# Kernel optimization log

Hardware: AMD Instinct MI355X
Metric: run time of the kernel (lower is better)

The kernel has to match this reference:

```python
import jax, jax.numpy as jnp
import numpy as np


def _window_indices(L, K):
    # 0-based (emo, cau) index pairs kept in the torch flattening order:
    # emo varies slowly (outer), cau varies fast (inner), |cau-emo| <= K.
    i = np.repeat(np.arange(L), L)
    j = np.tile(np.arange(L), L)
    m = np.abs(j - i) <= K
    return i[m], j[m]


def setup_inputs() -> dict:
    key = jax.random.key(0)
    ks = jax.random.split(key, 6)
    B, L, D = 4, 512, 768
    K, P = 10, 50
    R = 2 * D + P  # rank_feat_dim = 1586
    return {
        "doc_sents_h": jax.random.normal(ks[0], (B, L, D), jnp.float32),
        "pos_emb": jax.random.normal(ks[1], (2 * K + 1, P), jnp.float32) * 0.05,
        "W1": jax.random.normal(ks[2], (R, R), jnp.float32) * (1.0 / np.sqrt(R)),
        "b1": jax.random.normal(ks[3], (R,), jnp.float32) * 0.01,
        "W2": jax.random.normal(ks[4], (R, 1), jnp.float32) * (1.0 / np.sqrt(R)),
        "b2": jax.random.normal(ks[5], (1,), jnp.float32) * 0.01,
    }


def reference(doc_sents_h, pos_emb, W1, b1, W2, b2):
    B, L, D = doc_sents_h.shape
    K = (pos_emb.shape[0] - 1) // 2
    ei, ci = _window_indices(L, K)           # static numpy, shape [n]
    rel = jnp.asarray(ci - ei)               # [n] in [-K, K]
    # windowed pair features, [B, n, 2D] (skips the O(L^2) materialization)
    P_pairs = jnp.concatenate([doc_sents_h[:, ei], doc_sents_h[:, ci]], axis=-1)
    emb = pos_emb[rel + K]                   # [n, pos_dim]
    relf = rel.astype(pos_emb.dtype)
    kernel = jnp.exp(-jnp.square(relf[:, None] - relf[None, :]))  # [n, n]
    emb = kernel @ emb                       # [n, pos_dim], batch-invariant
    couples = jnp.concatenate(
        [P_pairs, jnp.broadcast_to(emb, (B,) + emb.shape)], axis=-1)  # [B, n, R]
    h = jax.nn.relu(couples @ W1 + b1)       # [B, n, R]
    pred = (h @ W2 + b2)[..., 0]             # [B, n]
    emo_cau_pos = jnp.stack(
        [jnp.asarray(ei) + 1, jnp.asarray(ci) + 1], axis=1)  # [n, 2], 1-based
    return pred, emo_cau_pos, h
```

## Files before the change

### kernel.cpp

```cpp
#include <hip/hip_runtime.h>
#include <math.h>

#define B_   4
#define L_   512
#define D_   768
#define K_   10
#define P_   50
#define R_   1586
#define NP_  10642
#define MROWS 2048
#define NPAD 1664
#define UVS  1600

#define PRED_OFF 0
#define POS_OFF  (B_ * NP_)
#define H_OFF    (B_ * NP_ + NP_ * 2)

typedef __attribute__((ext_vector_type(8))) short short8;
typedef __attribute__((ext_vector_type(4))) float floatx4;

__device__ __forceinline__ unsigned short f2bf(float f) {
    union { float f; unsigned int u; } a; a.f = f;
    unsigned int u = a.u;
    return (unsigned short)((u + 0x7FFF + ((u >> 16) & 1)) >> 16);
}
__device__ __forceinline__ float bf2f(unsigned short u) {
    union { unsigned int u; float f; } a; a.u = ((unsigned int)u) << 16;
    return a.f;
}

__device__ __forceinline__ int pair_offset(int i) {
    int h = i < K_ ? i : K_;
    int off = h * (K_ + 1) + (h * (h - 1)) / 2;
    if (i > K_) {
        int fullEnd = i < (L_ - K_) ? i : (L_ - K_);
        off += (fullEnd - K_) * (2 * K_ + 1);
        if (i > L_ - K_) {
            int t = i - (L_ - K_);
            int first = 2 * K_;
            int last = L_ + K_ - (i - 1);
            off += (first + last) * t / 2;
        }
    }
    return off;
}

__global__ __launch_bounds__(256) void convert_A(
        const float* __restrict__ doc, unsigned short* __restrict__ At) {
    int idx = (blockIdx.x * 256 + threadIdx.x) * 4;
    float4 v = *(const float4*)(doc + idx);
    ushort4 o;
    o.x = f2bf(v.x); o.y = f2bf(v.y); o.z = f2bf(v.z); o.w = f2bf(v.w);
    *(ushort4*)(At + idx) = o;
}

__global__ __launch_bounds__(256) void convert_W(
        const float* __restrict__ W1, unsigned short* __restrict__ Wt) {
    int z = blockIdx.z;
    int k0 = blockIdx.x * 32;
    int n0 = blockIdx.y * 32;
    __shared__ float tile[32][33];
    int tx = threadIdx.x & 31, ty = threadIdx.x >> 5;
    #pragma unroll
    for (int r = 0; r < 4; ++r) {
        int k = k0 + ty + r * 8;
        int n = n0 + tx;
        tile[ty + r * 8][tx] = (n < R_) ? W1[(size_t)(z * D_ + k) * R_ + n] : 0.f;
    }
    __syncthreads();
    #pragma unroll
    for (int r = 0; r < 4; ++r) {
        int n = n0 + ty + r * 8;
        int k = k0 + tx;
        Wt[(size_t)z * NPAD * D_ + (size_t)n * D_ + k] = f2bf(tile[tx][ty + r * 8]);
    }
}

__global__ __launch_bounds__(256) void build_F(
        const float* __restrict__ pos_emb, const float* __restrict__ W1,
        const float* __restrict__ b1, unsigned short* __restrict__ Fb) {
    int s = blockIdx.x;
    __shared__ float Es[P_];
    if (threadIdx.x < P_) {
        float acc = 0.f;
        #pragma unroll
        for (int r = 0; r <= 2 * K_; ++r) {
            float cnt = (float)(L_ - (r > K_ ? r - K_ : K_ - r));
            float d = (float)(s - r);
            acc += cnt * expf(-d * d) * pos_emb[r * P_ + threadIdx.x];
        }
        Es[threadIdx.x] = acc;
    }
    __syncthreads();
    for (int j = threadIdx.x; j < R_; j += blockDim.x) {
        float acc = b1[j];
        #pragma unroll 10
        for (int p = 0; p < P_; ++p)
            acc += Es[p] * W1[(2 * D_ + p) * R_ + j];
        Fb[s * UVS + j] = f2bf(acc);
    }
}

#define GLOAD_LDS16(g, l) __builtin_amdgcn_global_load_lds( \
    (const __attribute__((address_space(1))) void*)(g), \
    (__attribute__((address_space(3))) void*)(l), 16, 0, 0)

__global__ __launch_bounds__(256) void gemm_mfma(
        const unsigned short* __restrict__ At,
        const unsigned short* __restrict__ Wt,
        unsigned short* __restrict__ U, unsigned short* __restrict__ V) {
    __shared__ unsigned short Alds[128 * 32];
    __shared__ unsigned short Blds[128 * 32];
    const int tileN = blockIdx.x * 128;
    const int tileM = blockIdx.y * 128;
    const unsigned short* Bt = Wt + (size_t)blockIdx.z * NPAD * D_;
    unsigned short* C = blockIdx.z ? V : U;

    const int lane = threadIdx.x & 63;
    const int w = threadIdx.x >> 6;
    const int wm = (w & 1) * 64, wn = (w >> 1) * 64;
    const int quad = lane >> 4, l16 = lane & 15;

    floatx4 acc[4][4] = {};

    for (int k0 = 0; k0 < D_; k0 += 32) {
        #pragma unroll
        for (int t = 0; t < 2; ++t) {
            int g = (t * 4 + w) * 64 + lane;
            int m = g >> 2, c = g & 3;
            GLOAD_LDS16(At + (size_t)(tileM + m) * D_ + k0 + c * 8,
                        Alds + (t * 4 + w) * 512);
            GLOAD_LDS16(Bt + (size_t)(tileN + m) * D_ + k0 + c * 8,
                        Blds + (t * 4 + w) * 512);
        }
        __syncthreads();
        short8 a[4], b[4];
        #pragma unroll
        for (int im = 0; im < 4; ++im)
            a[im] = *(const short8*)&Alds[(wm + im * 16 + l16) * 32 + quad * 8];
        #pragma unroll
        for (int in = 0; in < 4; ++in)
            b[in] = *(const short8*)&Blds[(wn + in * 16 + l16) * 32 + quad * 8];
        #pragma unroll
        for (int im = 0; im < 4; ++im)
            #pragma unroll
            for (int in = 0; in < 4; ++in)
                acc[im][in] = __builtin_amdgcn_mfma_f32_16x16x32_bf16(
                    a[im], b[in], acc[im][in], 0, 0, 0);
        __syncthreads();
    }
    #pragma unroll
    for (int im = 0; im < 4; ++im) {
        #pragma unroll
        for (int in = 0; in < 4; ++in) {
            int col = tileN + wn + in * 16 + l16;
            if (col < R_) {
                #pragma unroll
                for (int r = 0; r < 4; ++r) {
                    int row = tileM + wm + im * 16 + quad * 4 + r;
                    C[(size_t)row * UVS + col] = f2bf(acc[im][in][r]);
                }
            }
        }
    }
}

#define NC2 13
__global__ __launch_bounds__(256) void epilogue(
        const unsigned short* __restrict__ U, const unsigned short* __restrict__ V,
        const unsigned short* __restrict__ Fb, const float* __restrict__ W2,
        const float* __restrict__ b2, float* __restrict__ out) {
    const int w    = threadIdx.x >> 6;
    const int lane = threadIdx.x & 63;
    const int i    = blockIdx.x * 4 + w;
    const int b    = blockIdx.y;
    const int half = blockIdx.z;

    const ushort2* u2  = (const ushort2*)(U + (size_t)(b * L_ + i) * UVS);
    const float2*  w2v = (const float2*)W2;

    float2 ur[NC2], wr[NC2];
    #pragma unroll
    for (int t = 0; t < NC2; ++t) {
        int c = lane + t * 64;
        if (c < R_ / 2) {
            ushort2 uu = u2[c];
            ur[t] = make_float2(bf2f(uu.x), bf2f(uu.y));
            wr[t] = w2v[c];
        }
    }

    const int base = i - K_ > 0 ? i - K_ : 0;
    const int poff = pair_offset(i);
    const float bias = b2[0];
    const int dj0 = half ? 11 : 0;
    const int dj1 = half ? 21 : 11;

    for (int dj = dj0; dj < dj1; ++dj) {
        int j = i - K_ + dj;
        if (j < 0 || j >= L_) continue;
        int p = poff + (j - base);
        const ushort2* v2 = (const ushort2*)(V + (size_t)(b * L_ + j) * UVS);
        const ushort2* f2 = (const ushort2*)(Fb + (size_t)dj * UVS);
        double* h2 = (double*)(out + H_OFF + (size_t)(b * NP_ + p) * R_);

        float acc = 0.f;
        #pragma unroll
        for (int t = 0; t < NC2; ++t) {
            int c = lane + t * 64;
            if (c < R_ / 2) {
                ushort2 vv = v2[c], ff = f2[c];
                float h0 = fmaxf(ur[t].x + bf2f(vv.x) + bf2f(ff.x), 0.f);
                float h1 = fmaxf(ur[t].y + bf2f(vv.y) + bf2f(ff.y), 0.f);
                union { float2 f; double d; } pk;
                pk.f = make_float2(h0, h1);
                __builtin_nontemporal_store(pk.d, h2 + c);
                acc += h0 * wr[t].x + h1 * wr[t].y;
            }
        }
        #pragma unroll
        for (int off = 32; off; off >>= 1) acc += __shfl_down(acc, off, 64);
        if (lane == 0) {
            out[PRED_OFF + b * NP_ + p] = acc + bias;
            if (b == 0) {
                out[POS_OFF + p * 2 + 0] = (float)(i + 1);
                out[POS_OFF + p * 2 + 1] = (float)(j + 1);
            }
        }
    }
}

extern "C" void kernel_launch(void* const* d_in, const int* in_sizes, int n_in,
                              void* d_out, int out_size, void* d_ws, size_t ws_size,
                              hipStream_t stream) {
    const float* doc     = (const float*)d_in[0];
    const float* pos_emb = (const float*)d_in[1];
    const float* W1      = (const float*)d_in[2];
    const float* b1      = (const float*)d_in[3];
    const float* W2      = (const float*)d_in[4];
    const float* b2      = (const float*)d_in[5];
    float* out = (float*)d_out;

    char* ws = (char*)d_ws;
    size_t off = 0;
    unsigned short* U  = (unsigned short*)(ws + off); off += (size_t)MROWS * UVS * 2;
    unsigned short* V  = (unsigned short*)(ws + off); off += (size_t)MROWS * UVS * 2;
    unsigned short* Fb = (unsigned short*)(ws + off); off += (size_t)21 * UVS * 2;
    off = (off + 255) & ~(size_t)255;
    unsigned short* At = (unsigned short*)(ws + off); off += (size_t)MROWS * D_ * 2;
    off = (off + 255) & ~(size_t)255;
    unsigned short* Wt = (unsigned short*)(ws + off);

    convert_A<<<MROWS * D_ / 1024, 256, 0, stream>>>(doc, At);
    convert_W<<<dim3(D_ / 32, NPAD / 32, 2), 256, 0, stream>>>(W1, Wt);
    build_F<<<21, 256, 0, stream>>>(pos_emb, W1, b1, Fb);
    gemm_mfma<<<dim3(NPAD / 128, MROWS / 128, 2), 256, 0, stream>>>(At, Wt, U, V);
    epilogue<<<dim3(L_ / 4, B_, 2), 256, 0, stream>>>(U, V, Fb, W2, b2, out);
}
```

Measured before the change: 372.7 us.

## Merge prep kernels, double-buffer GEMM LDS, widen epilogue loads

Folds the three preprocessing kernels (A conversion, W transpose-convert, positional bias build) into one launch, which removes two launch gaps. The GEMM now double-buffers its LDS tiles so the next K-slice is fetched while the current one feeds the MFMAs. The epilogue reads 16-byte vectors (8 bf16) instead of ushort2 and drops the z-split, so each wave handles all 21 window offsets. This gives fewer, wider memory transactions but halves the epilogue grid. The prefetch relies on the single end-of-iteration barrier to protect the buffer being overwritten.

```diff
diff --git a/kernel.cpp b/kernel.cpp
--- a/kernel.cpp
+++ b/kernel.cpp
@@ -45,42 +45,47 @@
     return off;
 }
 
-__global__ __launch_bounds__(256) void convert_A(
-        const float* __restrict__ doc, unsigned short* __restrict__ At) {
-    int idx = (blockIdx.x * 256 + threadIdx.x) * 4;
-    float4 v = *(const float4*)(doc + idx);
-    ushort4 o;
-    o.x = f2bf(v.x); o.y = f2bf(v.y); o.z = f2bf(v.z); o.w = f2bf(v.w);
-    *(ushort4*)(At + idx) = o;
-}
-
-__global__ __launch_bounds__(256) void convert_W(
-        const float* __restrict__ W1, unsigned short* __restrict__ Wt) {
-    int z = blockIdx.z;
-    int k0 = blockIdx.x * 32;
-    int n0 = blockIdx.y * 32;
+#define CA_BLOCKS 1536
+#define CW_BLOCKS 2496
+__global__ __launch_bounds__(256) void prep(
+        const float* __restrict__ doc, const float* __restrict__ pos_emb,
+        const float* __restrict__ W1, const float* __restrict__ b1,
+        unsigned short* __restrict__ At, unsigned short* __restrict__ Wt,
+        unsigned short* __restrict__ Fb) {
     __shared__ float tile[32][33];
-    int tx = threadIdx.x & 31, ty = threadIdx.x >> 5;
-    #pragma unroll
-    for (int r = 0; r < 4; ++r) {
-        int k = k0 + ty + r * 8;
-        int n = n0 + tx;
-        tile[ty + r * 8][tx] = (n < R_) ? W1[(size_t)(z * D_ + k) * R_ + n] : 0.f;
-    }
-    __syncthreads();
-    #pragma unroll
-    for (int r = 0; r < 4; ++r) {
-        int n = n0 + ty + r * 8;
-        int k = k0 + tx;
-        Wt[(size_t)z * NPAD * D_ + (size_t)n * D_ + k] = f2bf(tile[tx][ty + r * 8]);
-    }
-}
-
-__global__ __launch_bounds__(256) void build_F(
-        const float* __restrict__ pos_emb, const float* __restrict__ W1,
-        const float* __restrict__ b1, unsigned short* __restrict__ Fb) {
-    int s = blockIdx.x;
     __shared__ float Es[P_];
+    const int bid = blockIdx.x;
+
+    if (bid < CA_BLOCKS) {
+        int idx = (bid * 256 + threadIdx.x) * 4;
+        float4 v = *(const float4*)(doc + idx);
+        ushort4 o;
+        o.x = f2bf(v.x); o.y = f2bf(v.y); o.z = f2bf(v.z); o.w = f2bf(v.w);
+        *(ushort4*)(At + idx) = o;
+        return;
+    }
+    if (bid < CA_BLOCKS + CW_BLOCKS) {
+        int bb = bid - CA_BLOCKS;
+        int z = bb / 1248, rem = bb % 1248;
+        int k0 = (rem % 24) * 32;
+        int n0 = (rem / 24) * 32;
+        int tx = threadIdx.x & 31, ty = threadIdx.x >> 5;
+        #pragma unroll
+        for (int r = 0; r < 4; ++r) {
+            int k = k0 + ty + r * 8;
+            int n = n0 + tx;
+            tile[ty + r * 8][tx] = (n < R_) ? W1[(size_t)(z * D_ + k) * R_ + n] : 0.f;
+        }
+        __syncthreads();
+        #pragma unroll
+        for (int r = 0; r < 4; ++r) {
+            int n = n0 + ty + r * 8;
+            int k = k0 + tx;
+            Wt[(size_t)z * NPAD * D_ + (size_t)n * D_ + k] = f2bf(tile[tx][ty + r * 8]);
+        }
+        return;
+    }
+    int s = bid - (CA_BLOCKS + CW_BLOCKS);
     if (threadIdx.x < P_) {
         float acc = 0.f;
         #pragma unroll
@@ -92,7 +97,7 @@
         Es[threadIdx.x] = acc;
     }
     __syncthreads();
-    for (int j = threadIdx.x; j < R_; j += blockDim.x) {
+    for (int j = threadIdx.x; j < R_; j += 256) {
         float acc = b1[j];
         #pragma unroll 10
         for (int p = 0; p < P_; ++p)
@@ -109,8 +114,8 @@
         const unsigned short* __restrict__ At,
         const unsigned short* __restrict__ Wt,
         unsigned short* __restrict__ U, unsigned short* __restrict__ V) {
-    __shared__ unsigned short Alds[128 * 32];
-    __shared__ unsigned short Blds[128 * 32];
+    __shared__ unsigned short Alds[2][128 * 32];
+    __shared__ unsigned short Blds[2][128 * 32];
     const int tileN = blockIdx.x * 128;
     const int tileM = blockIdx.y * 128;
     const unsigned short* Bt = Wt + (size_t)blockIdx.z * NPAD * D_;
@@ -123,24 +128,30 @@
 
     floatx4 acc[4][4] = {};
 
+#define STAGE(buf, kk) do { \
+        _Pragma("unroll") \
+        for (int t = 0; t < 2; ++t) { \
+            int g = (t * 4 + w) * 64 + lane; \
+            int m = g >> 2, c = g & 3; \
+            GLOAD_LDS16(At + (size_t)(tileM + m) * D_ + (kk) + c * 8, \
+                        &Alds[buf][(t * 4 + w) * 512]); \
+            GLOAD_LDS16(Bt + (size_t)(tileN + m) * D_ + (kk) + c * 8, \
+                        &Blds[buf][(t * 4 + w) * 512]); \
+        } } while (0)
+
+    STAGE(0, 0);
+    __syncthreads();
+
+    int cur = 0;
     for (int k0 = 0; k0 < D_; k0 += 32) {
-        #pragma unroll
-        for (int t = 0; t < 2; ++t) {
-            int g = (t * 4 + w) * 64 + lane;
-            int m = g >> 2, c = g & 3;
-            GLOAD_LDS16(At + (size_t)(tileM + m) * D_ + k0 + c * 8,
-                        Alds + (t * 4 + w) * 512);
-            GLOAD_LDS16(Bt + (size_t)(tileN + m) * D_ + k0 + c * 8,
-                        Blds + (t * 4 + w) * 512);
-        }
-        __syncthreads();
+        if (k0 + 32 < D_) STAGE(cur ^ 1, k0 + 32);
         short8 a[4], b[4];
         #pragma unroll
         for (int im = 0; im < 4; ++im)
-            a[im] = *(const short8*)&Alds[(wm + im * 16 + l16) * 32 + quad * 8];
+            a[im] = *(const short8*)&Alds[cur][(wm + im * 16 + l16) * 32 + quad * 8];
         #pragma unroll
         for (int in = 0; in < 4; ++in)
-            b[in] = *(const short8*)&Blds[(wn + in * 16 + l16) * 32 + quad * 8];
+            b[in] = *(const short8*)&Blds[cur][(wn + in * 16 + l16) * 32 + quad * 8];
         #pragma unroll
         for (int im = 0; im < 4; ++im)
             #pragma unroll
@@ -148,7 +159,10 @@
                 acc[im][in] = __builtin_amdgcn_mfma_f32_16x16x32_bf16(
                     a[im], b[in], acc[im][in], 0, 0, 0);
         __syncthreads();
-    }
+        cur ^= 1;
+    }
+#undef STAGE
+
     #pragma unroll
     for (int im = 0; im < 4; ++im) {
         #pragma unroll
@@ -165,7 +179,7 @@
     }
 }
 
-#define NC2 13
+#define NG 4
 __global__ __launch_bounds__(256) void epilogue(
         const unsigned short* __restrict__ U, const unsigned short* __restrict__ V,
         const unsigned short* __restrict__ Fb, const float* __restrict__ W2,
@@ -174,48 +188,70 @@
     const int lane = threadIdx.x & 63;
     const int i    = blockIdx.x * 4 + w;
     const int b    = blockIdx.y;
-    const int half = blockIdx.z;
-
-    const ushort2* u2  = (const ushort2*)(U + (size_t)(b * L_ + i) * UVS);
-    const float2*  w2v = (const float2*)W2;
-
-    float2 ur[NC2], wr[NC2];
+
+    const unsigned short* urow = U + (size_t)(b * L_ + i) * UVS;
+
+    float uf[NG][8], wf[NG][8];
     #pragma unroll
-    for (int t = 0; t < NC2; ++t) {
-        int c = lane + t * 64;
-        if (c < R_ / 2) {
-            ushort2 uu = u2[c];
-            ur[t] = make_float2(bf2f(uu.x), bf2f(uu.y));
-            wr[t] = w2v[c];
+    for (int t = 0; t < NG; ++t) {
+        int g = lane + t * 64;
+        if (g < 198) {
+            short8 uu = *(const short8*)(urow + 8 * g);
+            float4 wa = *(const float4*)(W2 + 8 * g);
+            float4 wb = *(const float4*)(W2 + 8 * g + 4);
+            #pragma unroll
+            for (int e = 0; e < 8; ++e) uf[t][e] = bf2f((unsigned short)uu[e]);
+            wf[t][0] = wa.x; wf[t][1] = wa.y; wf[t][2] = wa.z; wf[t][3] = wa.w;
+            wf[t][4] = wb.x; wf[t][5] = wb.y; wf[t][6] = wb.z; wf[t][7] = wb.w;
+        } else if (g == 198) {
+            ushort2 uu = *(const ushort2*)(urow + 1584);
+            float2 wt = *(const float2*)(W2 + 1584);
+            uf[t][0] = bf2f(uu.x); uf[t][1] = bf2f(uu.y);
+            wf[t][0] = wt.x;       wf[t][1] = wt.y;
         }
     }
 
     const int base = i - K_ > 0 ? i - K_ : 0;
     const int poff = pair_offset(i);
     const float bias = b2[0];
-    const int dj0 = half ? 11 : 0;
-    const int dj1 = half ? 21 : 11;
-
-    for (int dj = dj0; dj < dj1; ++dj) {
+
+    for (int dj = 0; dj < 2 * K_ + 1; ++dj) {
         int j = i - K_ + dj;
-        if (j < 0 || j >= L_) continue;
+        if ((unsigned)j >= L_) continue;
         int p = poff + (j - base);
-        const ushort2* v2 = (const ushort2*)(V + (size_t)(b * L_ + j) * UVS);
-        const ushort2* f2 = (const ushort2*)(Fb + (size_t)dj * UVS);
+        const unsigned short* vrow = V + (size_t)(b * L_ + j) * UVS;
+        const unsigned short* frow = Fb + (size_t)dj * UVS;
         double* h2 = (double*)(out + H_OFF + (size_t)(b * NP_ + p) * R_);
 
         float acc = 0.f;
         #pragma unroll
-        for (int t = 0; t < NC2; ++t) {
-            int c = lane + t * 64;
-            if (c < R_ / 2) {
-                ushort2 vv = v2[c], ff = f2[c];
-                float h0 = fmaxf(ur[t].x + bf2f(vv.x) + bf2f(ff.x), 0.f);
-                float h1 = fmaxf(ur[t].y + bf2f(vv.y) + bf2f(ff.y), 0.f);
+        for (int t = 0; t < NG; ++t) {
+            int g = lane + t * 64;
+            if (g < 198) {
+                short8 vv = *(const short8*)(vrow + 8 * g);
+                short8 ff = *(const short8*)(frow + 8 * g);
+                float h[8];
+                #pragma unroll
+                for (int e = 0; e < 8; ++e) {
+                    h[e] = fmaxf(uf[t][e] + bf2f((unsigned short)vv[e])
+                                          + bf2f((unsigned short)ff[e]), 0.f);
+                    acc += h[e] * wf[t][e];
+                }
+                #pragma unroll
+                for (int q = 0; q < 4; ++q) {
+                    union { float2 f; double d; } pk;
+                    pk.f = make_float2(h[2 * q], h[2 * q + 1]);
+                    __builtin_nontemporal_store(pk.d, h2 + 4 * g + q);
+                }
+            } else if (g == 198) {
+                ushort2 vv = *(const ushort2*)(vrow + 1584);
+                ushort2 ff = *(const ushort2*)(frow + 1584);
+                float h0 = fmaxf(uf[t][0] + bf2f(vv.x) + bf2f(ff.x), 0.f);
+                float h1 = fmaxf(uf[t][1] + bf2f(vv.y) + bf2f(ff.y), 0.f);
                 union { float2 f; double d; } pk;
                 pk.f = make_float2(h0, h1);
-                __builtin_nontemporal_store(pk.d, h2 + c);
-                acc += h0 * wr[t].x + h1 * wr[t].y;
+                __builtin_nontemporal_store(pk.d, h2 + 792);
+                acc += h0 * wf[t][0] + h1 * wf[t][1];
             }
         }
         #pragma unroll
@@ -251,9 +287,8 @@
     off = (off + 255) & ~(size_t)255;
     unsigned short* Wt = (unsigned short*)(ws + off);
 
-    convert_A<<<MROWS * D_ / 1024, 256, 0, stream>>>(doc, At);
-    convert_W<<<dim3(D_ / 32, NPAD / 32, 2), 256, 0, stream>>>(W1, Wt);
-    build_F<<<21, 256, 0, stream>>>(pos_emb, W1, b1, Fb);
+    prep<<<CA_BLOCKS + CW_BLOCKS + 21, 256, 0, stream>>>(
+        doc, pos_emb, W1, b1, At, Wt, Fb);
     gemm_mfma<<<dim3(NPAD / 128, MROWS / 128, 2), 256, 0, stream>>>(At, Wt, U, V);
-    epilogue<<<dim3(L_ / 4, B_, 2), 256, 0, stream>>>(U, V, Fb, W2, b2, out);
-}
+    epilogue<<<dim3(L_ / 4, B_), 256, 0, stream>>>(U, V, Fb, W2, b2, out);
+}
```

Result: slower. 454.2 us (+21.9%).
